# Performance work log

Measured on AMD Instinct MI355X. Metric: run time of the kernel, lower is better.

The kernel has to match this reference:

```python
import jax, jax.numpy as jnp
from jax import lax
import numpy as np


def _hermite(x):
    """First n Hermite polynomials (physicists') evaluated at x of shape (..., n, 1).

    Three-term recurrence H_k = 2*x*H_{k-1} - 2*(k-1)*H_{k-2}, expressed as a
    lax.scan so the sequential state stays fused instead of n unrolled ops.
    Returns shape (..., n, n) with entry (..., i, j) = H_j(x_i).
    """
    n = x.shape[-2]
    H0 = jnp.ones_like(x)
    if n == 1:
        return H0
    H1 = 2.0 * x
    if n == 2:
        return jnp.concatenate([H0, H1], axis=-1)
    coeffs = 2.0 * jnp.arange(1, n - 1, dtype=x.dtype)  # 2*(k-1) for k = 2..n-1

    def step(carry, c):
        Hm1, Hm2 = carry
        Hk = 2.0 * x * Hm1 - c * Hm2
        return (Hk, Hm1), Hk

    _, Hs = lax.scan(step, (H1, H0), coeffs)  # (n-2, ..., n, 1)
    Hs = jnp.moveaxis(Hs[..., 0], 0, -1)      # (..., n, n-2)
    return jnp.concatenate([H0, H1, Hs], axis=-1)  # (..., n, n)


def setup_inputs() -> dict:
    key = jax.random.key(0)
    x = jax.random.normal(key, (65536, 32, 1), dtype=jnp.float32)
    # Dense(1) kernel initialized to [[sqrt(omega_init)]] with omega_init = 1.0
    omega_kernel = jnp.ones((1, 1), dtype=jnp.float32)
    return {"x": x, "omega_kernel": omega_kernel}


def reference(x, omega_kernel):
    # Dense(1, use_bias=False): sqrt_omega_x = x @ kernel, shape (..., n, 1)
    s = jnp.matmul(x, omega_kernel)
    hermite_polys = _hermite(s)                 # (..., n, n)
    gaussian_envelopes = jnp.exp(-jnp.square(s) / 2.0)  # (..., n, 1)
    return gaussian_envelopes * hermite_polys   # (..., n, n)
```

## Files before the change

### kernel.cpp

```cpp
#include <hip/hip_runtime.h>
#include <hip/hip_bf16.h>


#define KPT 8

typedef float f32x4 __attribute__((ext_vector_type(4)));

template <bool GUARD>
__global__ __launch_bounds__(256) void hoo_kernel(
    const float* __restrict__ x,
    const float* __restrict__ omega,
    f32x4* __restrict__ out4,
    unsigned n_quads)
{
    const unsigned tid  = threadIdx.x;
    const unsigned quad = tid & 7;
    const unsigned base = blockIdx.x * (256u * KPT) + tid;

    const float k = omega[0];

    float env[KPT], twox[KPT];
    float h0[KPT], h1[KPT], h2[KPT], h3[KPT];

#pragma unroll
    for (int kk = 0; kk < KPT; ++kk) {
        const unsigned f   = base + (unsigned)kk * 256u;
        const unsigned row = (GUARD ? (f < n_quads ? f : n_quads - 1u) : f) >> 3;
        const float s = x[row] * k;
        env[kk]  = __expf(-0.5f * (s * s));
        const float tx = 2.0f * s;
        twox[kk] = tx;
        h0[kk] = 1.0f;
        h1[kk] = tx;
        h2[kk] = tx * h1[kk] - 2.0f;
        h3[kk] = tx * h2[kk] - 4.0f * h1[kk];
    }

    float c = 6.0f;
    for (unsigned it = 0; it < quad; ++it) {
        const float c1 = c + 2.0f;
        const float c2 = c + 4.0f;
        const float c3 = c + 6.0f;
#pragma unroll
        for (int kk = 0; kk < KPT; ++kk) {
            const float tx = twox[kk];
            const float n0 = tx * h3[kk] - c  * h2[kk];
            const float n1 = tx * n0     - c1 * h3[kk];
            const float n2 = tx * n1     - c2 * n0;
            const float n3 = tx * n2     - c3 * n1;
            h0[kk] = n0; h1[kk] = n1; h2[kk] = n2; h3[kk] = n3;
        }
        c += 8.0f;
    }

#pragma unroll
    for (int kk = 0; kk < KPT; ++kk) {
        const unsigned f = base + (unsigned)kk * 256u;
        if (!GUARD || f < n_quads) {
            f32x4 v;
            v.x = env[kk] * h0[kk];
            v.y = env[kk] * h1[kk];
            v.z = env[kk] * h2[kk];
            v.w = env[kk] * h3[kk];
            out4[f] = v;
        }
    }
}

extern "C" void kernel_launch(void* const* d_in, const int* in_sizes, int n_in,
                              void* d_out, int out_size, void* d_ws, size_t ws_size,
                              hipStream_t stream) {
    const float* x     = (const float*)d_in[0];
    const float* omega = (const float*)d_in[1];
    f32x4* out4        = (f32x4*)d_out;

    const unsigned n_rows  = (unsigned)in_sizes[0];
    const unsigned n_quads = n_rows * 8u;

    const unsigned spb = 256u * KPT;
    const unsigned grid = (n_quads + spb - 1) / spb;

    if (n_quads % spb == 0) {
        hoo_kernel<false><<<grid, 256, 0, stream>>>(x, omega, out4, n_quads);
    } else {
        hoo_kernel<true><<<grid, 256, 0, stream>>>(x, omega, out4, n_quads);
    }
}
```

Before: 47.63 us.

## Convert to persistent grid-stride loop with prefetch of next tile's inputs

The grid is capped at 2048 blocks, and each block loops over tiles with a grid stride. While it computes the current tile it prefetches the x values for the next tile into registers. This is meant to hide input load latency and cut block launch overhead. The trade-offs are higher register pressure and less parallelism if the grid cap underfills the GPU. Output is a 64 MB write-bound stream, so the gain may be small.

After: 52.29 us. +9.8%, slower.

```diff
diff --git a/kernel.cpp b/kernel.cpp
--- a/kernel.cpp
+++ b/kernel.cpp
@@ -3,6 +3,7 @@
 
 
 #define KPT 8
+#define NBLK 2048
 
 typedef float f32x4 __attribute__((ext_vector_type(4)));
 
@@ -11,59 +12,84 @@
     const float* __restrict__ x,
     const float* __restrict__ omega,
     f32x4* __restrict__ out4,
-    unsigned n_quads)
+    unsigned n_quads,
+    unsigned stride)
 {
     const unsigned tid  = threadIdx.x;
     const unsigned quad = tid & 7;
-    const unsigned base = blockIdx.x * (256u * KPT) + tid;
-
     const float k = omega[0];
 
-    float env[KPT], twox[KPT];
-    float h0[KPT], h1[KPT], h2[KPT], h3[KPT];
+    unsigned base = blockIdx.x * (256u * KPT) + tid;
 
+    float sv[KPT];
 #pragma unroll
     for (int kk = 0; kk < KPT; ++kk) {
         const unsigned f   = base + (unsigned)kk * 256u;
         const unsigned row = (GUARD ? (f < n_quads ? f : n_quads - 1u) : f) >> 3;
-        const float s = x[row] * k;
-        env[kk]  = __expf(-0.5f * (s * s));
-        const float tx = 2.0f * s;
-        twox[kk] = tx;
-        h0[kk] = 1.0f;
-        h1[kk] = tx;
-        h2[kk] = tx * h1[kk] - 2.0f;
-        h3[kk] = tx * h2[kk] - 4.0f * h1[kk];
+        sv[kk] = x[row];
     }
 
-    float c = 6.0f;
-    for (unsigned it = 0; it < quad; ++it) {
-        const float c1 = c + 2.0f;
-        const float c2 = c + 4.0f;
-        const float c3 = c + 6.0f;
+    while (true) {
+        const unsigned next = base + stride;
+        const bool have_next = next < n_quads;
+
+        float s_cur[KPT];
+#pragma unroll
+        for (int kk = 0; kk < KPT; ++kk) s_cur[kk] = sv[kk];
+        if (have_next) {
+#pragma unroll
+            for (int kk = 0; kk < KPT; ++kk) {
+                const unsigned f   = next + (unsigned)kk * 256u;
+                const unsigned row = (GUARD ? (f < n_quads ? f : n_quads - 1u) : f) >> 3;
+                sv[kk] = x[row];
+            }
+        }
+
+        float env[KPT], twox[KPT], h0[KPT], h1[KPT], h2[KPT], h3[KPT];
 #pragma unroll
         for (int kk = 0; kk < KPT; ++kk) {
-            const float tx = twox[kk];
-            const float n0 = tx * h3[kk] - c  * h2[kk];
-            const float n1 = tx * n0     - c1 * h3[kk];
-            const float n2 = tx * n1     - c2 * n0;
-            const float n3 = tx * n2     - c3 * n1;
-            h0[kk] = n0; h1[kk] = n1; h2[kk] = n2; h3[kk] = n3;
+            const float s = s_cur[kk] * k;
+            env[kk] = __expf(-0.5f * (s * s));
+            const float tx = 2.0f * s;
+            twox[kk] = tx;
+            h0[kk] = 1.0f;
+            h1[kk] = tx;
+            h2[kk] = tx * tx - 2.0f;
+            h3[kk] = tx * h2[kk] - 4.0f * tx;
         }
-        c += 8.0f;
-    }
+
+        float c = 6.0f;
+        for (unsigned it = 0; it < quad; ++it) {
+            const float c1 = c + 2.0f;
+            const float c2 = c + 4.0f;
+            const float c3 = c + 6.0f;
+#pragma unroll
+            for (int kk = 0; kk < KPT; ++kk) {
+                const float tx = twox[kk];
+                const float n0 = tx * h3[kk] - c  * h2[kk];
+                const float n1 = tx * n0     - c1 * h3[kk];
+                const float n2 = tx * n1     - c2 * n0;
+                const float n3 = tx * n2     - c3 * n1;
+                h0[kk] = n0; h1[kk] = n1; h2[kk] = n2; h3[kk] = n3;
+            }
+            c += 8.0f;
+        }
 
 #pragma unroll
-    for (int kk = 0; kk < KPT; ++kk) {
-        const unsigned f = base + (unsigned)kk * 256u;
-        if (!GUARD || f < n_quads) {
-            f32x4 v;
-            v.x = env[kk] * h0[kk];
-            v.y = env[kk] * h1[kk];
-            v.z = env[kk] * h2[kk];
-            v.w = env[kk] * h3[kk];
-            out4[f] = v;
+        for (int kk = 0; kk < KPT; ++kk) {
+            const unsigned f = base + (unsigned)kk * 256u;
+            if (!GUARD || f < n_quads) {
+                f32x4 v;
+                v.x = env[kk] * h0[kk];
+                v.y = env[kk] * h1[kk];
+                v.z = env[kk] * h2[kk];
+                v.w = env[kk] * h3[kk];
+                out4[f] = v;
+            }
         }
+
+        if (!have_next) break;
+        base = next;
     }
 }
 
@@ -78,11 +104,13 @@
     const unsigned n_quads = n_rows * 8u;
 
     const unsigned spb = 256u * KPT;
-    const unsigned grid = (n_quads + spb - 1) / spb;
+    const unsigned blocks_needed = (n_quads + spb - 1) / spb;
+    const unsigned grid = blocks_needed < NBLK ? blocks_needed : NBLK;
+    const unsigned stride = grid * spb;
 
     if (n_quads % spb == 0) {
-        hoo_kernel<false><<<grid, 256, 0, stream>>>(x, omega, out4, n_quads);
+        hoo_kernel<false><<<grid, 256, 0, stream>>>(x, omega, out4, n_quads, stride);
     } else {
-        hoo_kernel<true><<<grid, 256, 0, stream>>>(x, omega, out4, n_quads);
+        hoo_kernel<true><<<grid, 256, 0, stream>>>(x, omega, out4, n_quads, stride);
     }
 }
```
